# Optimization experiments

Hardware: AMD Instinct MI355X
Metric: run time of the kernel (lower is better)

## Reference

```python
import jax, jax.numpy as jnp
import numpy as np

HID = 1024
NH = 16
HD = HID // NH  # 64


def _lin_params(key, fan_in, fan_out):
    k1, k2 = jax.random.split(key)
    lim = 1.0 / np.sqrt(fan_in)
    W = jax.random.uniform(k1, (fan_in, fan_out), jnp.float32, -lim, lim)
    b = jax.random.uniform(k2, (fan_out,), jnp.float32, -lim, lim)
    return W, b


def setup_inputs() -> dict:
    key = jax.random.key(0)
    ks = jax.random.split(key, 12)
    B, S = 4, 1024
    inp = {
        'query': jax.random.normal(ks[0], (B, S, HID), jnp.float32),
        'key': jax.random.normal(ks[1], (B, S, HID), jnp.float32),
        'value': jax.random.normal(ks[2], (B, S, HID), jnp.float32),
    }
    inp['Wq'], inp['bq'] = _lin_params(ks[3], HID, HID)
    inp['Wk'], inp['bk'] = _lin_params(ks[4], HID, HID)
    inp['Wv'], inp['bv'] = _lin_params(ks[5], HID, HID)
    inp['Wp'], inp['bp'] = _lin_params(ks[6], HID, HID)
    inp['Wup'], inp['bup'] = _lin_params(ks[7], HD, 1)
    inp['Wud'], inp['bud'] = _lin_params(ks[8], HD, 1)
    inp['Wus'], inp['bus'] = _lin_params(ks[9], HID, NH)
    inp['Wo'], inp['bo'] = _lin_params(ks[10], HID, HID)
    return inp


def _split_heads(x, B, S):
    # [B,S,HID] -> [B,NH,S,HD]
    return x.reshape(B, S, NH, HD).transpose(0, 2, 1, 3)


def reference(query, key, value, Wq, bq, Wk, bk, Wv, bv, Wp, bp,
              Wup, bup, Wud, bud, Wus, bus, Wo, bo):
    B, S, _ = query.shape
    len_q = S

    q = query @ Wq + bq   # [B,S,HID]
    k = key @ Wk + bk
    v = value @ Wv + bv

    # Gaussian-window positional bias (per head, per query position)
    p = _split_heads(q @ Wp + bp, B, S)              # [B,NH,S,HD]
    tp = jnp.tanh(p)
    p_i = tp @ Wup + bup                             # [B,NH,S,1]
    z_i = tp @ Wud + bud                             # [B,NH,S,1]
    cen_pos = len_q * jax.nn.sigmoid(p_i)            # [B,NH,S,1]
    win_size = len_q * jax.nn.sigmoid(z_i)           # [B,NH,S,1]
    pos = jnp.arange(len_q, dtype=q.dtype)[None, None, None, :]  # [1,1,1,S]
    bias = (pos - cen_pos) ** 2 / (0.5 * win_size ** 2)          # [B,NH,S,S]

    # per-head alpha gate from raw query
    alpha = jax.nn.sigmoid(query @ Wus + bus)        # [B,S,NH]
    alpha = alpha.reshape(B, S, NH, 1).transpose(0, 2, 1, 3)  # [B,NH,S,1]

    qh = _split_heads(q, B, S)
    kh = _split_heads(k, B, S)
    vh = _split_heads(v, B, S)

    scale = 1.0 / jnp.sqrt(jnp.asarray(HD, q.dtype))
    scores = jnp.einsum('bhqd,bhkd->bhqk', qh, kh) * scale
    scores = scores - alpha * bias                   # inject gated Gaussian bias
    attn = jax.nn.softmax(scores, axis=-1)           # [B,NH,S,S]

    out = jnp.einsum('bhqk,bhkd->bhqd', attn, vh)    # [B,NH,S,HD]
    x = out.transpose(0, 2, 1, 3).reshape(B, S, HID)
    x = x @ Wo + bo
    return x, attn
```

## Files before the change

### kernel.cpp

```cpp
#include <hip/hip_runtime.h>
#include <hip/hip_bf16.h>
#include <math.h>

#define S_LEN 1024
#define HIDN  1024
#define NHEAD 16
#define HDIM  64
#define BATCH 4
#define MTOT  (BATCH * S_LEN)

typedef __attribute__((ext_vector_type(8))) short          bf16v8;
typedef __attribute__((ext_vector_type(8))) unsigned short u16v8;
typedef __attribute__((ext_vector_type(4))) unsigned short u16v4;
typedef __attribute__((ext_vector_type(4))) float          f32v4;

__device__ __forceinline__ unsigned short f2bf_rne(float x) {
    unsigned int u = __float_as_uint(x);
    unsigned int r = (u + 0x7fffu + ((u >> 16) & 1u)) >> 16;
    return (unsigned short)r;
}
__device__ __forceinline__ float bf2f(unsigned short h) {
    return __uint_as_float(((unsigned int)h) << 16);
}
__device__ __forceinline__ void split2(float x, unsigned short& h, unsigned short& l) {
    h = f2bf_rne(x);
    l = f2bf_rne(x - bf2f(h));
}

__global__ __launch_bounds__(256) void split_w4(
    const float* __restrict__ W0, const float* __restrict__ W1,
    const float* __restrict__ W2, const float* __restrict__ W3,
    unsigned short* __restrict__ Hbase, unsigned short* __restrict__ Lbase)
{
    __shared__ float T[64][65];
    const int t  = threadIdx.x;
    const int k0 = blockIdx.y * 64;
    const int n0 = blockIdx.x * 64;
    const int z  = blockIdx.z;
    const float* W = (z == 0) ? W0 : (z == 1) ? W1 : (z == 2) ? W2 : W3;
    unsigned short* H = Hbase + (size_t)z * 1024 * 1024;
    unsigned short* L = Lbase + (size_t)z * 1024 * 1024;

    const int r = t >> 4;
    const int c = (t & 15) * 4;
#pragma unroll
    for (int i = 0; i < 4; ++i) {
        const int rr = r + i * 16;
        const float4 v = *(const float4*)&W[(size_t)(k0 + rr) * 1024 + n0 + c];
        T[rr][c + 0] = v.x; T[rr][c + 1] = v.y;
        T[rr][c + 2] = v.z; T[rr][c + 3] = v.w;
    }
    __syncthreads();

    const int n  = t >> 2;
    const int ko = (t & 3) * 16;
    u16v8 h0, h1, l0, l1;
#pragma unroll
    for (int kk = 0; kk < 8; ++kk) {
        unsigned short hh, ll;
        split2(T[ko + kk][n], hh, ll);
        h0[kk] = hh; l0[kk] = ll;
    }
#pragma unroll
    for (int kk = 0; kk < 8; ++kk) {
        unsigned short hh, ll;
        split2(T[ko + 8 + kk][n], hh, ll);
        h1[kk] = hh; l1[kk] = ll;
    }
    unsigned short* Hp = &H[(size_t)(n0 + n) * 1024 + k0 + ko];
    unsigned short* Lp = &L[(size_t)(n0 + n) * 1024 + k0 + ko];
    *(u16v8*)(Hp)     = h0;
    *(u16v8*)(Hp + 8) = h1;
    *(u16v8*)(Lp)     = l0;
    *(u16v8*)(Lp + 8) = l1;
}

__global__ __launch_bounds__(256) void alpha_kernel(
    const float* __restrict__ X, const float* __restrict__ Wus,
    const float* __restrict__ bus, float* __restrict__ alpha)
{
    __shared__ float Ws[1024 * 16];
    const int t = threadIdx.x;
#pragma unroll
    for (int i = 0; i < 16; ++i) {
        const int idx = t + i * 256;
        *reinterpret_cast<float4*>(&Ws[idx * 4]) =
            *reinterpret_cast<const float4*>(&Wus[idx * 4]);
    }
    __syncthreads();

    const int r = t >> 4, c = t & 15;
    const size_t row = (size_t)blockIdx.x * 16 + r;
    const float* x = &X[row * 1024];
    float acc = 0.f;
    for (int kk = 0; kk < 1024; kk += 4) {
        const float4 xv = *reinterpret_cast<const float4*>(&x[kk]);
        acc = fmaf(xv.x, Ws[(kk + 0) * 16 + c], acc);
        acc = fmaf(xv.y, Ws[(kk + 1) * 16 + c], acc);
        acc = fmaf(xv.z, Ws[(kk + 2) * 16 + c], acc);
        acc = fmaf(xv.w, Ws[(kk + 3) * 16 + c], acc);
    }
    acc += bus[c];
    alpha[row * 16 + c] = 1.f / (1.f + expf(-acc));
}

template<int AF32, int EPI>
__global__ __launch_bounds__(512, 2) void gemm_t(
    const float* __restrict__ Af,
    const unsigned short* __restrict__ Ah, const unsigned short* __restrict__ Al,
    const unsigned short* __restrict__ Bh, const unsigned short* __restrict__ Bl,
    const float* __restrict__ bias, float* __restrict__ Cf,
    unsigned short* __restrict__ Ch, unsigned short* __restrict__ Cl,
    const float* __restrict__ Wup, const float* __restrict__ Wud,
    const float* __restrict__ bup, const float* __restrict__ bud,
    const float* __restrict__ alpha, float* __restrict__ cenp,
    float* __restrict__ c0p)
{
    __shared__ short Ash[128][72];
    __shared__ short Asl[128][72];
    __shared__ short Bsh[64][72];
    __shared__ short Bsl[64][72];
    __shared__ float PSUP[2][128], PSUD[2][128];

    const int t    = threadIdx.x;
    const int bm   = blockIdx.y * 128;
    const int bn   = blockIdx.x * 64;
    const int lane = t & 63;
    const int wid  = t >> 6;
    const int wr   = wid >> 1;
    const int wc   = wid & 1;
    const int fr   = lane & 15;
    const int fq   = lane >> 4;

    f32v4 zero = {0.f, 0.f, 0.f, 0.f};
    f32v4 acc[2][2];
#pragma unroll
    for (int i = 0; i < 2; ++i)
#pragma unroll
        for (int j = 0; j < 2; ++j) acc[i][j] = zero;

    const int sra = t >> 2;
    const int sca = (t & 3) * 16;
    const int tb  = t & 255;
    const int srb = tb >> 2;
    const int scb = (tb & 3) * 16;
    const bool isBl = (t >= 256);
    const unsigned short* pB = isBl ? &Bl[(size_t)(bn + srb) * 1024 + scb]
                                    : &Bh[(size_t)(bn + srb) * 1024 + scb];
    const float* pAf = AF32 ? &Af[(size_t)(bm + sra) * 1024 + sca] : nullptr;
    const unsigned short* pAh = AF32 ? nullptr : &Ah[(size_t)(bm + sra) * 1024 + sca];
    const unsigned short* pAl = AF32 ? nullptr : &Al[(size_t)(bm + sra) * 1024 + sca];

    u16v8 rah0, rah1, ral0, ral1, rb0, rb1;
    auto LOAD = [&](int k0) {
        if (AF32) {
            const float4 a0 = *(const float4*)(pAf + k0);
            const float4 a1 = *(const float4*)(pAf + k0 + 4);
            const float4 a2 = *(const float4*)(pAf + k0 + 8);
            const float4 a3 = *(const float4*)(pAf + k0 + 12);
            const float xs[16] = {a0.x, a0.y, a0.z, a0.w, a1.x, a1.y, a1.z, a1.w,
                                  a2.x, a2.y, a2.z, a2.w, a3.x, a3.y, a3.z, a3.w};
#pragma unroll
            for (int e = 0; e < 8; ++e) {
                unsigned short hh, ll;
                split2(xs[e], hh, ll);
                rah0[e] = hh; ral0[e] = ll;
            }
#pragma unroll
            for (int e = 0; e < 8; ++e) {
                unsigned short hh, ll;
                split2(xs[8 + e], hh, ll);
                rah1[e] = hh; ral1[e] = ll;
            }
        } else {
            rah0 = *(const u16v8*)(pAh + k0);
            rah1 = *(const u16v8*)(pAh + k0 + 8);
            ral0 = *(const u16v8*)(pAl + k0);
            ral1 = *(const u16v8*)(pAl + k0 + 8);
        }
        rb0 = *(const u16v8*)(pB + k0);
        rb1 = *(const u16v8*)(pB + k0 + 8);
    };

    LOAD(0);
    for (int k0 = 0; k0 < 1024; k0 += 64) {
        __syncthreads();
        *(u16v8*)&Ash[sra][sca]     = rah0;
        *(u16v8*)&Ash[sra][sca + 8] = rah1;
        *(u16v8*)&Asl[sra][sca]     = ral0;
        *(u16v8*)&Asl[sra][sca + 8] = ral1;
        if (isBl) {
            *(u16v8*)&Bsl[srb][scb]     = rb0;
            *(u16v8*)&Bsl[srb][scb + 8] = rb1;
        } else {
            *(u16v8*)&Bsh[srb][scb]     = rb0;
            *(u16v8*)&Bsh[srb][scb + 8] = rb1;
        }
        __syncthreads();

        if (k0 + 64 < 1024) LOAD(k0 + 64);

#pragma unroll
        for (int kk2 = 0; kk2 < 2; ++kk2) {
            const int ks = kk2 * 32 + fq * 8;
            bf16v8 fah[2], fal[2], fbh[2], fbl[2];
#pragma unroll
            for (int i = 0; i < 2; ++i) {
                fah[i] = *(const bf16v8*)&Ash[wr * 32 + i * 16 + fr][ks];
                fal[i] = *(const bf16v8*)&Asl[wr * 32 + i * 16 + fr][ks];
            }
#pragma unroll
            for (int j = 0; j < 2; ++j) {
                fbh[j] = *(const bf16v8*)&Bsh[wc * 32 + j * 16 + fr][ks];
                fbl[j] = *(const bf16v8*)&Bsl[wc * 32 + j * 16 + fr][ks];
            }
#pragma unroll
            for (int i = 0; i < 2; ++i)
#pragma unroll
                for (int j = 0; j < 2; ++j) {
                    acc[i][j] = __builtin_amdgcn_mfma_f32_16x16x32_bf16(
                        fah[i], fbh[j], acc[i][j], 0, 0, 0);
                    acc[i][j] = __builtin_amdgcn_mfma_f32_16x16x32_bf16(
                        fah[i], fbl[j], acc[i][j], 0, 0, 0);
                    acc[i][j] = __builtin_amdgcn_mfma_f32_16x16x32_bf16(
                        fal[i], fbh[j], acc[i][j], 0, 0, 0);
                }
        }
    }

    if (EPI == 3) {
        float wupj[2], wudj[2], bb[2];
#pragma unroll
        for (int j = 0; j < 2; ++j) {
            const int colL = wc * 32 + j * 16 + fr;
            wupj[j] = Wup[colL];
            wudj[j] = Wud[colL];
            bb[j]   = bias[bn + colL];
        }
        float su[2][4], sd[2][4];
#pragma unroll
        for (int i = 0; i < 2; ++i)
#pragma unroll
            for (int r = 0; r < 4; ++r) { su[i][r] = 0.f; sd[i][r] = 0.f; }
#pragma unroll
        for (int j = 0; j < 2; ++j)
#pragma unroll
            for (int i = 0; i < 2; ++i)
#pragma unroll
                for (int r = 0; r < 4; ++r) {
                    const float tv = tanhf(acc[i][j][r] + bb[j]);
                    su[i][r] = fmaf(tv, wupj[j], su[i][r]);
                    sd[i][r] = fmaf(tv, wudj[j], sd[i][r]);
                }
#pragma unroll
        for (int i = 0; i < 2; ++i)
#pragma unroll
            for (int r = 0; r < 4; ++r) {
                float a = su[i][r], d = sd[i][r];
                a += __shfl_xor(a, 1); d += __shfl_xor(d, 1);
                a += __shfl_xor(a, 2); d += __shfl_xor(d, 2);
                a += __shfl_xor(a, 4); d += __shfl_xor(d, 4);
                a += __shfl_xor(a, 8); d += __shfl_xor(d, 8);
                if (fr == 0) {
                    const int row = wr * 32 + i * 16 + fq * 4 + r;
                    PSUP[wc][row] = a;
                    PSUD[wc][row] = d;
                }
            }
        __syncthreads();
        if (t < 128) {
            const float ap = PSUP[0][t] + PSUP[1][t] + bup[0];
            const float az = PSUD[0][t] + PSUD[1][t] + bud[0];
            const float cenv = 1024.f / (1.f + expf(-ap));
            const float win  = 1024.f / (1.f + expf(-az));
            const int grow = bm + t;
            const int hd   = bn >> 6;
            const int zz   = (grow >> 10) * 16 + hd;
            const int s    = grow & 1023;
            const float al = alpha[(size_t)grow * 16 + hd];
            cenp[(size_t)zz * 1024 + s] = cenv;
            c0p[(size_t)zz * 1024 + s]  = al * 2.f / (win * win);
        }
        return;
    }

#pragma unroll
    for (int j = 0; j < 2; ++j) {
        const int col = bn + wc * 32 + j * 16 + fr;
        const float bb = bias[col];
#pragma unroll
        for (int i = 0; i < 2; ++i) {
            const int row0 = bm + wr * 32 + i * 16 + fq * 4;
            const f32v4 cv = acc[i][j];
            if (EPI == 2) {
                u16v4 h4, l4;
#pragma unroll
                for (int r = 0; r < 4; ++r) {
                    unsigned short hh, ll;
                    split2(cv[r] + bb, hh, ll);
                    h4[r] = hh; l4[r] = ll;
                }
                const size_t base =
                    ((size_t)((row0 >> 10) * 16 + (col >> 6)) * 64 + (col & 63)) * 1024
                    + (row0 & 1023);
                *(u16v4*)&Ch[base] = h4;
                *(u16v4*)&Cl[base] = l4;
            } else if (EPI == 1) {
#pragma unroll
                for (int r = 0; r < 4; ++r) {
                    unsigned short hh, ll;
                    split2(cv[r] + bb, hh, ll);
                    const size_t idx = (size_t)(row0 + r) * 1024 + col;
                    Ch[idx] = hh; Cl[idx] = ll;
                }
            } else {
#pragma unroll
                for (int r = 0; r < 4; ++r)
                    Cf[(size_t)(row0 + r) * 1024 + col] = cv[r] + bb;
            }
        }
    }
}

#define M0_SHIFT 8.0f
__global__ __launch_bounds__(512, 2) void attn_fused(
    const unsigned short* __restrict__ qh, const unsigned short* __restrict__ ql,
    const unsigned short* __restrict__ kh, const unsigned short* __restrict__ kl,
    const unsigned short* __restrict__ vTh, const unsigned short* __restrict__ vTl,
    const float* __restrict__ cen, const float* __restrict__ c0,
    float* __restrict__ attn,
    unsigned short* __restrict__ oh, unsigned short* __restrict__ ol)
{
    __shared__ unsigned short KH[64][64], KL[64][64];
    __shared__ unsigned short VH[64][64], VL[64][64];
    __shared__ unsigned short PH[128][64], PL[128][64];
    __shared__ float CEN[128], C0S[128];
    __shared__ float LSUM[2][128];
    __shared__ float RINV[128];

    const int bid   = blockIdx.x;
    const int z     = ((bid >> 6) << 3) | (bid & 7);
    const int itile = (bid >> 3) & 7;
    const int i0    = itile * 128;
    const int bq    = z >> 4;
    const int hd    = z & 15;

    const int t    = threadIdx.x;
    const int lane = t & 63;
    const int wid  = t >> 6;
    const int wrp  = wid >> 1;
    const int wc   = wid & 1;
    const int fr   = lane & 15, fq = lane >> 4;

    if (t < 128) {
        CEN[t] = cen[(size_t)z * 1024 + i0 + t];
        C0S[t] = c0[(size_t)z * 1024 + i0 + t];
    }

    bf16v8 qfh_[2][2], qfl_[2][2];
#pragma unroll
    for (int i = 0; i < 2; ++i)
#pragma unroll
        for (int kk = 0; kk < 2; ++kk) {
            const size_t qa = (size_t)(bq * 1024 + i0 + wrp * 32 + i * 16 + fr) * 1024
                              + hd * 64 + kk * 32 + fq * 8;
            qfh_[i][kk] = *(const bf16v8*)&qh[qa];
            qfl_[i][kk] = *(const bf16v8*)&ql[qa];
        }

    float lsum[2][4];
#pragma unroll
    for (int i = 0; i < 2; ++i)
#pragma unroll
        for (int r = 0; r < 4; ++r) lsum[i][r] = 0.f;

    const f32v4 zero = {0.f, 0.f, 0.f, 0.f};

    const int srow = t >> 3;
    const int sseg = t & 7;
    const int ssl  = (sseg ^ (srow & 7)) * 8;
    const unsigned short* vhb = vTh + (size_t)z * 64 * 1024;
    const unsigned short* vlb = vTl + (size_t)z * 64 * 1024;

    u16v8 rkh, rkl, rvh, rvl;
    auto LOADK = [&](int j0) {
        const size_t ga = (size_t)(bq * 1024 + j0 + srow) * 1024 + hd * 64 + sseg * 8;
        rkh = *(const u16v8*)&kh[ga];
        rkl = *(const u16v8*)&kl[ga];
    };
    auto LOADV = [&](int j0) {
        const size_t va = (size_t)srow * 1024 + j0 + sseg * 8;
        rvh = *(const u16v8*)&vhb[va];
        rvl = *(const u16v8*)&vlb[va];
    };

    LOADK(0);
    for (int jt = 0; jt < 16; ++jt) {
        const int j0 = jt * 64;
        unsigned short (*KHc)[64] = (jt & 1) ? VH : KH;
        unsigned short (*KLc)[64] = (jt & 1) ? VL : KL;
        *(u16v8*)&KHc[srow][ssl] = rkh;
        *(u16v8*)&KLc[srow][ssl] = rkl;
        __syncthreads();
        if (jt < 15) LOADK(j0 + 64);

        f32v4 acc[2][2];
#pragma unroll
        for (int i = 0; i < 2; ++i)
#pragma unroll
            for (int j2 = 0; j2 < 2; ++j2) acc[i][j2] = zero;

        __builtin_amdgcn_s_setprio(1);
#pragma unroll
        for (int kk = 0; kk < 2; ++kk) {
            bf16v8 fbh[2], fbl[2];
#pragma unroll
            for (int j2 = 0; j2 < 2; ++j2) {
                const int rb = wc * 32 + j2 * 16 + fr;
                const int sb = ((kk * 4 + fq) ^ (rb & 7)) * 8;
                fbh[j2] = *(const bf16v8*)&KHc[rb][sb];
                fbl[j2] = *(const bf16v8*)&KLc[rb][sb];
            }
#pragma unroll
            for (int i = 0; i < 2; ++i)
#pragma unroll
                for (int j2 = 0; j2 < 2; ++j2) {
                    acc[i][j2] = __builtin_amdgcn_mfma_f32_16x16x32_bf16(
                        qfh_[i][kk], fbh[j2], acc[i][j2], 0, 0, 0);
                    acc[i][j2] = __builtin_amdgcn_mfma_f32_16x16x32_bf16(
                        qfh_[i][kk], fbl[j2], acc[i][j2], 0, 0, 0);
                    acc[i][j2] = __builtin_amdgcn_mfma_f32_16x16x32_bf16(
                        qfl_[i][kk], fbh[j2], acc[i][j2], 0, 0, 0);
                }
        }
        __builtin_amdgcn_s_setprio(0);

#pragma unroll
        for (int i = 0; i < 2; ++i)
#pragma unroll
            for (int r = 0; r < 4; ++r) {
                const int row = wrp * 32 + i * 16 + fq * 4 + r;
                const float cv = CEN[row], cc = C0S[row];
                float al = 0.f;
#pragma unroll
                for (int j2 = 0; j2 < 2; ++j2) {
                    const int col = wc * 32 + j2 * 16 + fr;
                    const float dd = (float)(j0 + col) - cv;
                    const float s  = acc[i][j2][r] * 0.125f - cc * dd * dd;
                    al += __expf(s - M0_SHIFT);
                }
                lsum[i][r] += al;
            }
    }

#pragma unroll
    for (int i = 0; i < 2; ++i)
#pragma unroll
        for (int r = 0; r < 4; ++r) {
            float v = lsum[i][r];
            v += __shfl_xor(v, 1);
            v += __shfl_xor(v, 2);
            v += __shfl_xor(v, 4);
            v += __shfl_xor(v, 8);
            if (fr == 0) LSUM[wc][wrp * 32 + i * 16 + fq * 4 + r] = v;
        }
    __syncthreads();
    if (t < 128) RINV[t] = 1.f / (LSUM[0][t] + LSUM[1][t]);

    f32v4 acco[2][2];
#pragma unroll
    for (int i = 0; i < 2; ++i)
#pragma unroll
        for (int j = 0; j < 2; ++j) acco[i][j] = zero;

    float* attnZ = attn + (size_t)z * 1024 * 1024;

    LOADK(0);
    LOADV(0);
    for (int jt = 0; jt < 16; ++jt) {
        const int j0 = jt * 64;
        __syncthreads();
        *(u16v8*)&KH[srow][ssl] = rkh;
        *(u16v8*)&KL[srow][ssl] = rkl;
        *(u16v8*)&VH[srow][ssl] = rvh;
        *(u16v8*)&VL[srow][ssl] = rvl;
        __syncthreads();
        if (jt < 15) { LOADK(j0 + 64); LOADV(j0 + 64); }

        f32v4 acc[2][2];
#pragma unroll
        for (int i = 0; i < 2; ++i)
#pragma unroll
            for (int j2 = 0; j2 < 2; ++j2) acc[i][j2] = zero;

        __builtin_amdgcn_s_setprio(1);
#pragma unroll
        for (int kk = 0; kk < 2; ++kk) {
            bf16v8 fbh[2], fbl[2];
#pragma unroll
            for (int j2 = 0; j2 < 2; ++j2) {
                const int rb = wc * 32 + j2 * 16 + fr;
                const int sb = ((kk * 4 + fq) ^ (rb & 7)) * 8;
                fbh[j2] = *(const bf16v8*)&KH[rb][sb];
                fbl[j2] = *(const bf16v8*)&KL[rb][sb];
            }
#pragma unroll
            for (int i = 0; i < 2; ++i)
#pragma unroll
                for (int j2 = 0; j2 < 2; ++j2) {
                    acc[i][j2] = __builtin_amdgcn_mfma_f32_16x16x32_bf16(
                        qfh_[i][kk], fbh[j2], acc[i][j2], 0, 0, 0);
                    acc[i][j2] = __builtin_amdgcn_mfma_f32_16x16x32_bf16(
                        qfh_[i][kk], fbl[j2], acc[i][j2], 0, 0, 0);
                    acc[i][j2] = __builtin_amdgcn_mfma_f32_16x16x32_bf16(
                        qfl_[i][kk], fbh[j2], acc[i][j2], 0, 0, 0);
                }
        }
        __builtin_amdgcn_s_setprio(0);

#pragma unroll
        for (int i = 0; i < 2; ++i)
#pragma unroll
            for (int r = 0; r < 4; ++r) {
                const int row = wrp * 32 + i * 16 + fq * 4 + r;
                const float cv = CEN[row], cc = C0S[row], ri = RINV[row];
#pragma unroll
                for (int j2 = 0; j2 < 2; ++j2) {
                    const int col = wc * 32 + j2 * 16 + fr;
                    const float dd = (float)(j0 + col) - cv;
                    const float s  = acc[i][j2][r] * 0.125f - cc * dd * dd;
                    const float p  = __expf(s - M0_SHIFT) * ri;
                    attnZ[(size_t)(i0 + row) * 1024 + j0 + col] = p;
                    unsigned short hv, lv;
                    split2(p, hv, lv);
                    const int slot = ((col >> 3) ^ (row & 7)) * 8 + (col & 7);
                    PH[row][slot] = hv;
                    PL[row][slot] = lv;
                }
            }
        __syncthreads();

        __builtin_amdgcn_s_setprio(1);
#pragma unroll
        for (int kk = 0; kk < 2; ++kk) {
            bf16v8 pah[2], pal[2], fbh[2], fbl[2];
#pragma unroll
            for (int iq = 0; iq < 2; ++iq) {
                const int rp = wrp * 32 + iq * 16 + fr;
                const int sp = ((kk * 4 + fq) ^ (rp & 7)) * 8;
                pah[iq] = *(const bf16v8*)&PH[rp][sp];
                pal[iq] = *(const bf16v8*)&PL[rp][sp];
            }
#pragma unroll
            for (int jd = 0; jd < 2; ++jd) {
                const int rb = wc * 32 + jd * 16 + fr;
                const int sb = ((kk * 4 + fq) ^ (rb & 7)) * 8;
                fbh[jd] = *(const bf16v8*)&VH[rb][sb];
                fbl[jd] = *(const bf16v8*)&VL[rb][sb];
            }
#pragma unroll
            for (int iq = 0; iq < 2; ++iq)
#pragma unroll
                for (int jd = 0; jd < 2; ++jd) {
                    acco[iq][jd] = __builtin_amdgcn_mfma_f32_16x16x32_bf16(
                        pah[iq], fbh[jd], acco[iq][jd], 0, 0, 0);
                    acco[iq][jd] = __builtin_amdgcn_mfma_f32_16x16x32_bf16(
                        pah[iq], fbl[jd], acco[iq][jd], 0, 0, 0);
                    acco[iq][jd] = __builtin_amdgcn_mfma_f32_16x16x32_bf16(
                        pal[iq], fbh[jd], acco[iq][jd], 0, 0, 0);
                }
        }
        __builtin_amdgcn_s_setprio(0);
    }

#pragma unroll
    for (int jd = 0; jd < 2; ++jd) {
        const int dcol = wc * 32 + jd * 16 + fr;
#pragma unroll
        for (int iq = 0; iq < 2; ++iq) {
            const int row0 = i0 + wrp * 32 + iq * 16 + fq * 4;
            const f32v4 cv = acco[iq][jd];
#pragma unroll
            for (int r = 0; r < 4; ++r) {
                unsigned short hv, lv;
                split2(cv[r], hv, lv);
                const size_t idx = (size_t)(bq * 1024 + row0 + r) * 1024 + hd * 64 + dcol;
                oh[idx] = hv;
                ol[idx] = lv;
            }
        }
    }
}

extern "C" void kernel_launch(void* const* d_in, const int* in_sizes, int n_in,
                              void* d_out, int out_size, void* d_ws, size_t ws_size,
                              hipStream_t stream)
{
    const float* query = (const float*)d_in[0];
    const float* key_  = (const float*)d_in[1];
    const float* value = (const float*)d_in[2];
    const float* Wq  = (const float*)d_in[3];
    const float* bq  = (const float*)d_in[4];
    const float* Wk  = (const float*)d_in[5];
    const float* bk  = (const float*)d_in[6];
    const float* Wv  = (const float*)d_in[7];
    const float* bv  = (const float*)d_in[8];
    const float* Wp  = (const float*)d_in[9];
    const float* bp  = (const float*)d_in[10];
    const float* Wup = (const float*)d_in[11];
    const float* bup = (const float*)d_in[12];
    const float* Wud = (const float*)d_in[13];
    const float* bud = (const float*)d_in[14];
    const float* Wus = (const float*)d_in[15];
    const float* bus = (const float*)d_in[16];
    const float* Wo  = (const float*)d_in[17];
    const float* bo  = (const float*)d_in[18];

    float* x_out = (float*)d_out;
    float* attn  = x_out + (size_t)MTOT * HIDN;

    char* wsb = (char*)d_ws;
    unsigned short* qh  = (unsigned short*)(wsb);
    unsigned short* ql  = (unsigned short*)(wsb + (8u  << 20));
    unsigned short* kh  = (unsigned short*)(wsb + (16u << 20));
    unsigned short* kl  = (unsigned short*)(wsb + (24u << 20));
    unsigned short* vTh = (unsigned short*)(wsb + (32u << 20));
    unsigned short* vTl = (unsigned short*)(wsb + (40u << 20));
    unsigned short* oh  = (unsigned short*)(wsb + (48u << 20));
    unsigned short* ol  = (unsigned short*)(wsb + (56u << 20));
    float* alpha_ws = (float*)(wsb + (64u << 20));
    float* cen_ws   = (float*)(wsb + (64u << 20) + (256u << 10));
    float* c0_ws    = (float*)(wsb + (64u << 20) + (512u << 10));
    unsigned short* wh = (unsigned short*)attn;
    unsigned short* wl = wh + (size_t)4 * 1024 * 1024;
    unsigned short* w2h = qh;
    unsigned short* w2l = ql;

    const dim3 blk(256);
    const dim3 blk512(512);
    const dim3 ggemm(HIDN / 64, MTOT / 128);
    const size_t WSTEP = (size_t)1024 * 1024;

    split_w4<<<dim3(16, 16, 4), blk, 0, stream>>>(Wq, Wk, Wv, Wp, wh, wl);
    alpha_kernel<<<dim3(MTOT / 16), blk, 0, stream>>>(query, Wus, bus, alpha_ws);
    gemm_t<1, 1><<<ggemm, blk512, 0, stream>>>(
        query, nullptr, nullptr, wh, wl, bq, nullptr, qh, ql,
        nullptr, nullptr, nullptr, nullptr, nullptr, nullptr, nullptr);
    gemm_t<1, 1><<<ggemm, blk512, 0, stream>>>(
        key_, nullptr, nullptr, wh + WSTEP, wl + WSTEP, bk, nullptr, kh, kl,
        nullptr, nullptr, nullptr, nullptr, nullptr, nullptr, nullptr);
    gemm_t<1, 2><<<ggemm, blk512, 0, stream>>>(
        value, nullptr, nullptr, wh + 2 * WSTEP, wl + 2 * WSTEP, bv,
        nullptr, vTh, vTl,
        nullptr, nullptr, nullptr, nullptr, nullptr, nullptr, nullptr);
    gemm_t<0, 3><<<ggemm, blk512, 0, stream>>>(
        nullptr, qh, ql, wh + 3 * WSTEP, wl + 3 * WSTEP, bp, nullptr,
        nullptr, nullptr,
        Wup, Wud, bup, bud, alpha_ws, cen_ws, c0_ws);
    attn_fused<<<dim3(512), blk512, 0, stream>>>(
        qh, ql, kh, kl, vTh, vTl, cen_ws, c0_ws, attn, oh, ol);
    split_w4<<<dim3(16, 16, 1), blk, 0, stream>>>(Wo, Wo, Wo, Wo, w2h, w2l);
    gemm_t<0, 0><<<ggemm, blk512, 0, stream>>>(
        nullptr, oh, ol, w2h, w2l, bo, x_out, nullptr, nullptr,
        nullptr, nullptr, nullptr, nullptr, nullptr, nullptr, nullptr);
}
```

Before: 368.1 us.

## Split PV over key halves per wave to drop a barrier, reduce via LDS

Each wave column now multiplies only the P columns it wrote (its own half of the key tile) against all 64 V columns, instead of reading P written by other waves. This removes the __syncthreads between writing P and the PV MFMAs. The two partial output accumulators are summed through LDS at the end. The cost is twice the accumulator registers per wave plus an extra LDS reduction in the epilogue. Correctness relies on each wave reading only the P columns it wrote itself, and on the barrier at the top of the next iteration to protect P/V reuse.

```diff
diff --git a/kernel.cpp b/kernel.cpp
--- a/kernel.cpp
+++ b/kernel.cpp
@@ -467,11 +467,11 @@
     __syncthreads();
     if (t < 128) RINV[t] = 1.f / (LSUM[0][t] + LSUM[1][t]);
 
-    f32v4 acco[2][2];
+    f32v4 acco[2][4];
 #pragma unroll
     for (int i = 0; i < 2; ++i)
 #pragma unroll
-        for (int j = 0; j < 2; ++j) acco[i][j] = zero;
+        for (int j = 0; j < 4; ++j) acco[i][j] = zero;
 
     float* attnZ = attn + (size_t)z * 1024 * 1024;
 
@@ -538,55 +538,72 @@
                     PL[row][slot] = lv;
                 }
             }
-        __syncthreads();
 
         __builtin_amdgcn_s_setprio(1);
-#pragma unroll
-        for (int kk = 0; kk < 2; ++kk) {
-            bf16v8 pah[2], pal[2], fbh[2], fbl[2];
+        {
+            bf16v8 pah[2], pal[2];
 #pragma unroll
             for (int iq = 0; iq < 2; ++iq) {
                 const int rp = wrp * 32 + iq * 16 + fr;
-                const int sp = ((kk * 4 + fq) ^ (rp & 7)) * 8;
+                const int sp = ((wc * 4 + fq) ^ (rp & 7)) * 8;
                 pah[iq] = *(const bf16v8*)&PH[rp][sp];
                 pal[iq] = *(const bf16v8*)&PL[rp][sp];
             }
 #pragma unroll
-            for (int jd = 0; jd < 2; ++jd) {
-                const int rb = wc * 32 + jd * 16 + fr;
-                const int sb = ((kk * 4 + fq) ^ (rb & 7)) * 8;
-                fbh[jd] = *(const bf16v8*)&VH[rb][sb];
-                fbl[jd] = *(const bf16v8*)&VL[rb][sb];
-            }
-#pragma unroll
-            for (int iq = 0; iq < 2; ++iq)
-#pragma unroll
-                for (int jd = 0; jd < 2; ++jd) {
+            for (int jd = 0; jd < 4; ++jd) {
+                const int rb = jd * 16 + fr;
+                const int sb = ((wc * 4 + fq) ^ (rb & 7)) * 8;
+                const bf16v8 vfh = *(const bf16v8*)&VH[rb][sb];
+                const bf16v8 vfl = *(const bf16v8*)&VL[rb][sb];
+#pragma unroll
+                for (int iq = 0; iq < 2; ++iq) {
                     acco[iq][jd] = __builtin_amdgcn_mfma_f32_16x16x32_bf16(
-                        pah[iq], fbh[jd], acco[iq][jd], 0, 0, 0);
+                        pah[iq], vfh, acco[iq][jd], 0, 0, 0);
                     acco[iq][jd] = __builtin_amdgcn_mfma_f32_16x16x32_bf16(
-                        pah[iq], fbl[jd], acco[iq][jd], 0, 0, 0);
+                        pah[iq], vfl, acco[iq][jd], 0, 0, 0);
                     acco[iq][jd] = __builtin_amdgcn_mfma_f32_16x16x32_bf16(
-                        pal[iq], fbh[jd], acco[iq][jd], 0, 0, 0);
-                }
+                        pal[iq], vfh, acco[iq][jd], 0, 0, 0);
+                }
+            }
         }
         __builtin_amdgcn_s_setprio(0);
     }
 
-#pragma unroll
-    for (int jd = 0; jd < 2; ++jd) {
-        const int dcol = wc * 32 + jd * 16 + fr;
-#pragma unroll
-        for (int iq = 0; iq < 2; ++iq) {
-            const int row0 = i0 + wrp * 32 + iq * 16 + fq * 4;
-            const f32v4 cv = acco[iq][jd];
+    __syncthreads();
+    if (wc == 1) {
+        float* s0 = (float*)PH;
+        float* s1 = (float*)PL;
+#pragma unroll
+        for (int jd = 0; jd < 4; ++jd)
 #pragma unroll
             for (int r = 0; r < 4; ++r) {
-                unsigned short hv, lv;
-                split2(cv[r], hv, lv);
-                const size_t idx = (size_t)(bq * 1024 + row0 + r) * 1024 + hd * 64 + dcol;
-                oh[idx] = hv;
-                ol[idx] = lv;
+                const int idx = ((wrp * 4 + jd) * 4 + r) * 64 + lane;
+                s0[idx] = acco[0][jd][r];
+                s1[idx] = acco[1][jd][r];
+            }
+    }
+    __syncthreads();
+    if (wc == 0) {
+        const float* s0 = (const float*)PH;
+        const float* s1 = (const float*)PL;
+#pragma unroll
+        for (int jd = 0; jd < 4; ++jd) {
+            const int dcol = jd * 16 + fr;
+#pragma unroll
+            for (int iq = 0; iq < 2; ++iq) {
+                const int row0 = i0 + wrp * 32 + iq * 16 + fq * 4;
+                const float* sp = (iq == 0) ? s0 : s1;
+#pragma unroll
+                for (int r = 0; r < 4; ++r) {
+                    const float v = acco[iq][jd][r] +
+                        sp[((wrp * 4 + jd) * 4 + r) * 64 + lane];
+                    unsigned short hv, lv;
+                    split2(v, hv, lv);
+                    const size_t idx = (size_t)(bq * 1024 + row0 + r) * 1024
+                                       + hd * 64 + dcol;
+                    oh[idx] = hv;
+                    ol[idx] = lv;
+                }
             }
         }
     }
```

New measurement: 368.2 us, median of 3. About the same (+0.0%).
